# Kernel tuning notes

Measured on AMD Instinct MI355X. Metric: run time of the kernel, lower is better.

The kernel has to match this reference:

```python
import jax, jax.numpy as jnp
import numpy as np

EPS = 1e-5  # torch BatchNorm2d default eps
K = 3       # kernel_size
D = 1       # dilation (== padding)


def setup_inputs() -> dict:
    key = jax.random.key(0)
    k0, k1, k2 = jax.random.split(key, 3)
    N, C, H, W, O = 4, 2048, 32, 32, 256
    return {
        "x": jax.random.normal(k0, (N, C, H, W), jnp.float32),
        "conv_w": jax.random.normal(k1, (K * K, C, K, K), jnp.float32) * 0.01,
        "gamma": jnp.ones((K * K,), jnp.float32),
        "beta": jnp.zeros((K * K,), jnp.float32),
        "weight": jax.random.normal(k2, (O, C, K * K), jnp.float32) * 0.01,
    }


def reference(x, conv_w, gamma, beta, weight):
    n, c, h, w = x.shape
    # --- dynamic-kernel generator: conv (stride 1, pad=dilation) -> BN (train mode) -> softmax over K*K ---
    sigma = jax.lax.conv_general_dilated(
        x, conv_w, window_strides=(1, 1), padding=[(D, D), (D, D)],
        rhs_dilation=(D, D), dimension_numbers=("NCHW", "OIHW", "NCHW"))  # (n, K*K, h, w)
    mean = sigma.mean(axis=(0, 2, 3), keepdims=True)
    var = sigma.var(axis=(0, 2, 3), keepdims=True)  # biased variance, as torch BN uses for normalization
    sigma = (sigma - mean) * jax.lax.rsqrt(var + EPS)
    sigma = sigma * gamma[None, :, None, None] + beta[None, :, None, None]
    sigma = jax.nn.softmax(sigma, axis=1)            # softmax over the K*K kernel positions
    sigma = sigma.reshape(n, K * K, h * w)           # (n, K*K, h*w)
    # --- unfold (im2col), channel-major (C, kh, kw) ordering matching torch F.unfold ---
    patches = jax.lax.conv_general_dilated_patches(
        x, (K, K), (1, 1), [(D, D), (D, D)], rhs_dilation=(D, D),
        dimension_numbers=("NCHW", "OIHW", "NCHW"))  # (n, C*K*K, h, w)
    patches = patches.reshape(n, c, K * K, h * w)     # (n, C, K*K, h*w)
    # --- per-pixel dynamic weighting + learned projection ---
    # out[n,o,m] = sum_{c,l} patches[n,c,l,m] * sigma[n,l,m] * weight[o,c,l]
    out = jnp.einsum("nclm,nlm,ocl->nom", patches, sigma, weight)
    return out.reshape(n, weight.shape[0], h, w)
```

## Files before the change

kernel.cpp:

```cpp
#include <hip/hip_runtime.h>
#include <hip/hip_bf16.h>
#include <stdint.h>

typedef unsigned short u16;
typedef __attribute__((ext_vector_type(8))) short short8;
typedef __attribute__((ext_vector_type(4))) float floatx4;

#define N_IMG 4
#define C_IN  2048
#define HW    1024
#define KK    9
#define O_OUT 256
#define NPIX  4096
#define M_PAD  2432
#define K_DIM  2048
#define BN_EPS 1e-5f

#define OFF_A    0u
#define OFF_XT   9961472u
#define OFF_H    26738688u
#define OFF_SRAW 46661632u
#define OFF_STAT 46809088u

__device__ __forceinline__ u16 f2b(float f) {
    unsigned u = __float_as_uint(f);
    return (u16)((u + 0x7FFFu + ((u >> 16) & 1u)) >> 16);
}

__device__ __forceinline__ void load8f(const float* base, size_t eidx, u16* out) {
    const float* p = base + eidx;
    float4 a = ((const float4*)p)[0];
    float4 b = ((const float4*)p)[1];
    float f[8] = {a.x, a.y, a.z, a.w, b.x, b.y, b.z, b.w};
#pragma unroll
    for (int j = 0; j < 8; ++j) out[j] = f2b(f[j]);
}

__global__ void build_all(const float* __restrict__ x, const float* __restrict__ wgt,
                          const float* __restrict__ cw, u16* __restrict__ xt,
                          u16* __restrict__ A, float* __restrict__ stats) {
    __shared__ __align__(16) u16 lds[9 * 2056];
    int b = blockIdx.x, t = threadIdx.x;
    if (b < 2048) {
        int c0 = (b & 31) * 64, p0 = ((b >> 5) & 15) * 64, n = b >> 9;
        int rp = t >> 3;
        int pv = (t & 7) * 8;
        u16 h0[8], h1[8];
        load8f(x, (size_t)(n * C_IN + c0 + 2 * rp) * HW + p0 + pv, h0);
        load8f(x, (size_t)(n * C_IN + c0 + 2 * rp + 1) * HW + p0 + pv, h1);
        unsigned* l32 = (unsigned*)lds;
#pragma unroll
        for (int j = 0; j < 8; ++j)
            l32[(pv + j) * 35 + rp] = (unsigned)h0[j] | ((unsigned)h1[j] << 16);
        __syncthreads();
        int pr = t >> 3, cq = (t & 7) * 4;
        unsigned o0[4], o1[4];
#pragma unroll
        for (int i = 0; i < 4; ++i) {
            o0[i] = l32[pr * 35 + cq + i];
            o1[i] = l32[(pr + 32) * 35 + cq + i];
        }
        *(uint4*)(xt + (size_t)(n * HW + p0 + pr) * K_DIM + c0 + cq * 2) = *(uint4*)o0;
        *(uint4*)(xt + (size_t)(n * HW + p0 + pr + 32) * K_DIM + c0 + cq * 2) = *(uint4*)o1;
    } else if (b < 2304) {
        int o = b - 2048;
        size_t base = (size_t)o * 18432;
        for (int i = 0; i < 9; ++i) {
            int e0 = (t + i * 256) * 8;
            u16 hv[8];
            load8f(wgt, base + e0, hv);
#pragma unroll
            for (int j = 0; j < 8; ++j) {
                int e = e0 + j;
                int c = e / 9, l = e - c * 9;
                lds[l * 2056 + c] = hv[j];
            }
        }
        __syncthreads();
        for (int l = 0; l < 9; ++l) {
            size_t row = (size_t)l * 256 + o;
            *(uint4*)(A + row * K_DIM + t * 8) = *(const uint4*)&lds[l * 2056 + t * 8];
        }
    } else if (b < 2313) {
        int l = b - 2304;
        size_t base = (size_t)l * 18432;
        for (int i = 0; i < 9; ++i) {
            int e0 = (t + i * 256) * 8;
            u16 hv[8];
            load8f(cw, base + e0, hv);
#pragma unroll
            for (int j = 0; j < 8; ++j) {
                int e = e0 + j;
                int c = e / 9, k = e - c * 9;
                lds[k * 2056 + c] = hv[j];
            }
        }
        __syncthreads();
        for (int k = 0; k < 9; ++k) {
            size_t row = 2304 + (size_t)k * 9 + l;
            *(uint4*)(A + row * K_DIM + t * 8) = *(const uint4*)&lds[k * 2056 + t * 8];
        }
    } else {
        uint4 z = {0, 0, 0, 0};
        uint4* dst = (uint4*)(A + (size_t)2385 * K_DIM);
        for (int i = t; i < (47 * 2048) / 8; i += 256) dst[i] = z;
        if (t < 18) stats[t] = 0.0f;
    }
}

__device__ __forceinline__ void gload_lds16(const void* g, void* l) {
    __builtin_amdgcn_global_load_lds((__attribute__((address_space(1))) void*)(g),
                                     (__attribute__((address_space(3))) void*)(l), 16, 0, 0);
}

__global__ void gemm_bt(const u16* __restrict__ A, const u16* __restrict__ B,
                        __hip_bfloat16* __restrict__ C) {
    __shared__ __align__(16) u16 As[2 * 128 * 32];
    __shared__ __align__(16) u16 Bs[2 * 128 * 32];
    int bx = blockIdx.x;
    int mt = bx % 19, nt = bx / 19;
    int m0 = mt * 128, n0 = nt * 128;
    int t = threadIdx.x;
    int w = t >> 6, lam = t & 63;
    int wm = w >> 1, wn = w & 1;
    int lm = lam & 15, q = lam >> 4;

    floatx4 acc[4][4];
    floatx4 z = {0.f, 0.f, 0.f, 0.f};
#pragma unroll
    for (int i = 0; i < 4; ++i)
#pragma unroll
        for (int j = 0; j < 4; ++j) acc[i][j] = z;

    int rsub = lam >> 2;
    int kc = (lam & 3) * 8;
    const u16* gA[4]; const u16* gB[4];
    u16* lA[4];       u16* lB[4];
#pragma unroll
    for (int ii = 0; ii < 4; ++ii) {
        int c = w * 4 + ii;
        int rc = c & 7, ks = c >> 3;
        gA[ii] = A + (size_t)(m0 + rc * 16 + rsub) * K_DIM + ks * 32 + kc;
        gB[ii] = B + (size_t)(n0 + rc * 16 + rsub) * K_DIM + ks * 32 + kc;
        lA[ii] = As + ks * 4096 + rc * 512;
        lB[ii] = Bs + ks * 4096 + rc * 512;
    }

    for (int kt = 0; kt < K_DIM / 64; ++kt) {
#pragma unroll
        for (int ii = 0; ii < 4; ++ii) {
            gload_lds16(gA[ii], lA[ii]);
            gload_lds16(gB[ii], lB[ii]);
            gA[ii] += 64; gB[ii] += 64;
        }
        __syncthreads();
#pragma unroll
        for (int ks = 0; ks < 2; ++ks) {
            short8 af[4], bf[4];
#pragma unroll
            for (int i = 0; i < 4; ++i)
                af[i] = *(const short8*)(As + ks * 4096 + (wm * 64 + i * 16 + lm) * 32 + q * 8);
#pragma unroll
            for (int j = 0; j < 4; ++j)
                bf[j] = *(const short8*)(Bs + ks * 4096 + (wn * 64 + j * 16 + lm) * 32 + q * 8);
#pragma unroll
            for (int i = 0; i < 4; ++i)
#pragma unroll
                for (int j = 0; j < 4; ++j)
                    acc[i][j] = __builtin_amdgcn_mfma_f32_16x16x32_bf16(af[i], bf[j], acc[i][j], 0, 0, 0);
        }
        __syncthreads();
    }
#pragma unroll
    for (int i = 0; i < 4; ++i) {
        int gm = m0 + wm * 64 + i * 16 + q * 4;
#pragma unroll
        for (int j = 0; j < 4; ++j) {
            int gn = n0 + wn * 64 + j * 16 + lm;
#pragma unroll
            for (int r = 0; r < 4; ++r)
                C[(size_t)(gm + r) * NPIX + gn] = __float2bfloat16(acc[i][j][r]);
        }
    }
}

__global__ void sigma_stats(const __hip_bfloat16* __restrict__ Hm, float* __restrict__ sraw,
                            float* __restrict__ stats) {
    int b = blockIdx.x;
    int qq = b & 3, nl = b >> 2;
    int n = nl / 9, l = nl - n * 9;
    int t = threadIdx.x;
    int pix = qq * 256 + t;
    int y = pix >> 5, x = pix & 31;
    float v = 0.f;
#pragma unroll
    for (int k = 0; k < 9; ++k) {
        int yy = y + k / 3 - 1, xx = x + (k % 3) - 1;
        if (yy >= 0 && yy < 32 && xx >= 0 && xx < 32)
            v += __bfloat162float(Hm[(size_t)(2304 + k * 9 + l) * NPIX + n * HW + yy * 32 + xx]);
    }
    sraw[(size_t)nl * HW + pix] = v;
    __shared__ float r1[256], r2[256];
    r1[t] = v; r2[t] = v * v;
    __syncthreads();
    for (int s = 128; s > 0; s >>= 1) {
        if (t < s) { r1[t] += r1[t + s]; r2[t] += r2[t + s]; }
        __syncthreads();
    }
    if (t == 0) { atomicAdd(&stats[l], r1[0]); atomicAdd(&stats[9 + l], r2[0]); }
}

__global__ void tail(const __hip_bfloat16* __restrict__ Hm, const float* __restrict__ sraw,
                     const float* __restrict__ stats, const float* __restrict__ gamma,
                     const float* __restrict__ beta, float* __restrict__ out) {
    int b = blockIdx.x;
    int n = b >> 8, rem = b & 255;
    int ph = rem >> 7, og = rem & 127;
    int t = threadIdx.x;
    float mean[9], istd[9], gg[9], bb[9];
#pragma unroll
    for (int l = 0; l < 9; ++l) {
        float m = stats[l] * (1.f / 4096.f);
        float var = stats[9 + l] * (1.f / 4096.f) - m * m;
        mean[l] = m; istd[l] = rsqrtf(var + BN_EPS);
        gg[l] = gamma[l]; bb[l] = beta[l];
    }
    const __hip_bfloat16* hb = Hm + (size_t)(og * 2) * NPIX + (size_t)n * HW;
    float* ob = out + ((size_t)n * 256 + og * 2) * HW;
#pragma unroll
    for (int i = 0; i < 2; ++i) {
        int pix = ph * 512 + i * 256 + t;
        int y = pix >> 5, x = pix & 31;
        float v[9];
        float mx = -1e30f;
#pragma unroll
        for (int l = 0; l < 9; ++l) {
            float tv = (sraw[(size_t)(n * 9 + l) * HW + pix] - mean[l]) * istd[l];
            tv = tv * gg[l] + bb[l];
            v[l] = tv; mx = fmaxf(mx, tv);
        }
        float ssum = 0.f;
#pragma unroll
        for (int l = 0; l < 9; ++l) { v[l] = __expf(v[l] - mx); ssum += v[l]; }
        float inv = 1.f / ssum;
        float acc0 = 0.f, acc1 = 0.f;
#pragma unroll
        for (int l = 0; l < 9; ++l) {
            int dy = l / 3 - 1, dx = l % 3 - 1;
            int yy = y + dy, xx = x + dx;
            if (yy >= 0 && yy < 32 && xx >= 0 && xx < 32) {
                float sv = v[l] * inv;
                size_t hidx = (size_t)(l * 256) * NPIX + (size_t)(pix + dy * 32 + dx);
                acc0 += sv * __bfloat162float(hb[hidx]);
                acc1 += sv * __bfloat162float(hb[hidx + NPIX]);
            }
        }
        ob[pix] = acc0;
        ob[HW + pix] = acc1;
    }
}

extern "C" void kernel_launch(void* const* d_in, const int* in_sizes, int n_in,
                              void* d_out, int out_size, void* d_ws, size_t ws_size,
                              hipStream_t stream) {
    const float* x     = (const float*)d_in[0];
    const float* cw    = (const float*)d_in[1];
    const float* gamma = (const float*)d_in[2];
    const float* beta  = (const float*)d_in[3];
    const float* wgt   = (const float*)d_in[4];

    char* ws = (char*)d_ws;
    u16*   Abuf = (u16*)(ws + OFF_A);
    u16*   XT   = (u16*)(ws + OFF_XT);
    u16*   Hm   = (u16*)(ws + OFF_H);
    float* sraw = (float*)(ws + OFF_SRAW);
    float* stats= (float*)(ws + OFF_STAT);

    build_all<<<2314, 256, 0, stream>>>(x, wgt, cw, XT, Abuf, stats);
    gemm_bt<<<19 * 32, 256, 0, stream>>>(Abuf, XT, (__hip_bfloat16*)Hm);
    sigma_stats<<<N_IMG * KK * 4, 256, 0, stream>>>((const __hip_bfloat16*)Hm, sraw, stats);
    tail<<<1024, 256, 0, stream>>>((const __hip_bfloat16*)Hm, sraw, stats, gamma, beta, (float*)d_out);
}
```

Measured before the change: 170.6 us.

## Rewrite GEMM with 256x256 tiles, swizzled LDS and ping-pong pipelined MFMA schedule

```diff
diff --git a/kernel.cpp b/kernel.cpp
--- a/kernel.cpp
+++ b/kernel.cpp
@@ -12,15 +12,16 @@
 #define KK    9
 #define O_OUT 256
 #define NPIX  4096
-#define M_PAD  2432
+#define M_PAD  2560
+#define H_ROWS 2432
 #define K_DIM  2048
 #define BN_EPS 1e-5f
 
 #define OFF_A    0u
-#define OFF_XT   9961472u
-#define OFF_H    26738688u
-#define OFF_SRAW 46661632u
-#define OFF_STAT 46809088u
+#define OFF_XT   10485760u
+#define OFF_H    27262976u
+#define OFF_SRAW 47185920u
+#define OFF_STAT 47333376u
 
 __device__ __forceinline__ u16 f2b(float f) {
     unsigned u = __float_as_uint(f);
@@ -113,73 +114,155 @@
                                      (__attribute__((address_space(3))) void*)(l), 16, 0, 0);
 }
 
-__global__ void gemm_bt(const u16* __restrict__ A, const u16* __restrict__ B,
-                        __hip_bfloat16* __restrict__ C) {
-    __shared__ __align__(16) u16 As[2 * 128 * 32];
-    __shared__ __align__(16) u16 Bs[2 * 128 * 32];
-    int bx = blockIdx.x;
-    int mt = bx % 19, nt = bx / 19;
-    int m0 = mt * 128, n0 = nt * 128;
+#define STG(gbase, ldsarr, bb, hh, kt) do {                                                        \
+    gload_lds16((gbase) + (size_t)((hh) * 128 + (w * 2 + 0) * 8) * K_DIM + (size_t)(kt) * 64,      \
+                (ldsarr) + (bb) * 16384 + (hh) * 8192 + ldsw);                                     \
+    gload_lds16((gbase) + (size_t)((hh) * 128 + (w * 2 + 1) * 8) * K_DIM + (size_t)(kt) * 64,      \
+                (ldsarr) + (bb) * 16384 + (hh) * 8192 + ldsw + 512);                               \
+} while (0)
+
+#define RD_A(bb, mi, ks) (*(const short8*)(As + (bb) * 16384 + arow + (mi) * 1024 + col[ks]))
+#define RD_B(bb, ni, ks) (*(const short8*)(Bs + (bb) * 16384 + brow + (ni) * 1024 + col[ks]))
+
+#define READ_BALL(bb) do {                                                   \
+    bq[0][0] = RD_B(bb, 0, 0); bq[0][1] = RD_B(bb, 0, 1);                    \
+    bq[1][0] = RD_B(bb, 1, 0); bq[1][1] = RD_B(bb, 1, 1);                    \
+    bq[2][0] = RD_B(bb, 2, 0); bq[2][1] = RD_B(bb, 2, 1);                    \
+    bq[3][0] = RD_B(bb, 3, 0); bq[3][1] = RD_B(bb, 3, 1);                    \
+} while (0)
+
+#define READ_AQ(bb, qd) do {                                                 \
+    aq[0][0] = RD_A(bb, 2 * (qd), 0);     aq[0][1] = RD_A(bb, 2 * (qd), 1);  \
+    aq[1][0] = RD_A(bb, 2 * (qd) + 1, 0); aq[1][1] = RD_A(bb, 2 * (qd) + 1, 1); \
+} while (0)
+
+#define MFMA1(mi, ni, ks) acc[mi][ni] = __builtin_amdgcn_mfma_f32_16x16x32_bf16( \
+    aq[(mi) & 1][ks], bq[ni][ks], acc[mi][ni], 0, 0, 0)
+
+#define MFMA_Q(qd) do {                                                                      \
+    MFMA1(2*(qd),   0, 0); MFMA1(2*(qd),   1, 0); MFMA1(2*(qd),   2, 0); MFMA1(2*(qd),   3, 0); \
+    MFMA1(2*(qd)+1, 0, 0); MFMA1(2*(qd)+1, 1, 0); MFMA1(2*(qd)+1, 2, 0); MFMA1(2*(qd)+1, 3, 0); \
+    MFMA1(2*(qd),   0, 1); MFMA1(2*(qd),   1, 1); MFMA1(2*(qd),   2, 1); MFMA1(2*(qd),   3, 1); \
+    MFMA1(2*(qd)+1, 0, 1); MFMA1(2*(qd)+1, 1, 1); MFMA1(2*(qd)+1, 2, 1); MFMA1(2*(qd)+1, 3, 1); \
+} while (0)
+
+#define BAR1_MFMA(qd) do {                                   \
+    __builtin_amdgcn_s_barrier();                            \
+    asm volatile("s_waitcnt lgkmcnt(0)" ::: "memory");       \
+    __builtin_amdgcn_sched_barrier(0);                       \
+    __builtin_amdgcn_s_setprio(1);                           \
+    MFMA_Q(qd);                                              \
+    __builtin_amdgcn_s_setprio(0);                           \
+} while (0)
+#define BAR2() __builtin_amdgcn_s_barrier()
+#define VMW4() asm volatile("s_waitcnt vmcnt(4)" ::: "memory")
+#define VMW0() asm volatile("s_waitcnt vmcnt(0)" ::: "memory")
+
+__global__ __launch_bounds__(512, 2) void gemm_bt(const u16* __restrict__ A,
+                                                  const u16* __restrict__ B,
+                                                  __hip_bfloat16* __restrict__ C) {
+    __shared__ __align__(16) u16 As[2 * 256 * 64];
+    __shared__ __align__(16) u16 Bs[2 * 256 * 64];
+
+    int orig = blockIdx.x;
+    int wgid = (orig & 7) * 20 + (orig >> 3);
+    int mt = wgid % 10, nt = wgid / 10;
+    int m0 = mt * 256, n0 = nt * 256;
+
     int t = threadIdx.x;
-    int w = t >> 6, lam = t & 63;
-    int wm = w >> 1, wn = w & 1;
-    int lm = lam & 15, q = lam >> 4;
-
-    floatx4 acc[4][4];
+    int w = t >> 6, L = t & 63;
+    int wm = w >> 2, wn = w & 3;
+    int q = L >> 4, lm = L & 15;
+    int lr = L >> 3, ls = L & 7;
+
+    int csw = (ls ^ lr) * 8;
+    const u16* gA0 = A + (size_t)(m0 + lr) * K_DIM + csw;
+    const u16* gB0 = B + (size_t)(n0 + lr) * K_DIM + csw;
+    int ldsw = w * 1024;
+
+    int sw = (lm & 7) << 3;
+    int arow = (wm * 128 + lm) * 64;
+    int brow = (wn * 64 + lm) * 64;
+    int col[2] = { (q * 8) ^ sw, (32 + q * 8) ^ sw };
+
+    floatx4 acc[8][4];
     floatx4 z = {0.f, 0.f, 0.f, 0.f};
 #pragma unroll
-    for (int i = 0; i < 4; ++i)
+    for (int i = 0; i < 8; ++i)
 #pragma unroll
         for (int j = 0; j < 4; ++j) acc[i][j] = z;
 
-    int rsub = lam >> 2;
-    int kc = (lam & 3) * 8;
-    const u16* gA[4]; const u16* gB[4];
-    u16* lA[4];       u16* lB[4];
-#pragma unroll
-    for (int ii = 0; ii < 4; ++ii) {
-        int c = w * 4 + ii;
-        int rc = c & 7, ks = c >> 3;
-        gA[ii] = A + (size_t)(m0 + rc * 16 + rsub) * K_DIM + ks * 32 + kc;
-        gB[ii] = B + (size_t)(n0 + rc * 16 + rsub) * K_DIM + ks * 32 + kc;
-        lA[ii] = As + ks * 4096 + rc * 512;
-        lB[ii] = Bs + ks * 4096 + rc * 512;
-    }
-
-    for (int kt = 0; kt < K_DIM / 64; ++kt) {
-#pragma unroll
-        for (int ii = 0; ii < 4; ++ii) {
-            gload_lds16(gA[ii], lA[ii]);
-            gload_lds16(gB[ii], lB[ii]);
-            gA[ii] += 64; gB[ii] += 64;
-        }
-        __syncthreads();
-#pragma unroll
-        for (int ks = 0; ks < 2; ++ks) {
-            short8 af[4], bf[4];
-#pragma unroll
-            for (int i = 0; i < 4; ++i)
-                af[i] = *(const short8*)(As + ks * 4096 + (wm * 64 + i * 16 + lm) * 32 + q * 8);
-#pragma unroll
-            for (int j = 0; j < 4; ++j)
-                bf[j] = *(const short8*)(Bs + ks * 4096 + (wn * 64 + j * 16 + lm) * 32 + q * 8);
-#pragma unroll
-            for (int i = 0; i < 4; ++i)
-#pragma unroll
-                for (int j = 0; j < 4; ++j)
-                    acc[i][j] = __builtin_amdgcn_mfma_f32_16x16x32_bf16(af[i], bf[j], acc[i][j], 0, 0, 0);
-        }
-        __syncthreads();
-    }
-#pragma unroll
-    for (int i = 0; i < 4; ++i) {
-        int gm = m0 + wm * 64 + i * 16 + q * 4;
-#pragma unroll
-        for (int j = 0; j < 4; ++j) {
-            int gn = n0 + wn * 64 + j * 16 + lm;
-#pragma unroll
-            for (int r = 0; r < 4; ++r)
-                C[(size_t)(gm + r) * NPIX + gn] = __float2bfloat16(acc[i][j][r]);
+    short8 aq[2][2], bq[4][2];
+
+    STG(gA0, As, 0, 0, 0); STG(gA0, As, 0, 1, 0);
+    STG(gB0, Bs, 0, 0, 0); STG(gB0, Bs, 0, 1, 0);
+    STG(gB0, Bs, 1, 0, 1); STG(gB0, Bs, 1, 1, 1);
+    VMW4();
+    BAR2();
+
+    for (int it = 0; it < 15; ++it) {
+        int T = 2 * it;
+        READ_BALL(0); READ_AQ(0, 0);
+        STG(gA0, As, 1, 0, T + 1); STG(gA0, As, 1, 1, T + 1);
+        BAR1_MFMA(0); BAR2();
+        READ_AQ(0, 1);
+        STG(gB0, Bs, 0, 0, T + 2);
+        BAR1_MFMA(1); BAR2();
+        READ_AQ(0, 2);
+        STG(gB0, Bs, 0, 1, T + 2);
+        BAR1_MFMA(2); BAR2();
+        READ_AQ(0, 3);
+        BAR1_MFMA(3); VMW4(); BAR2();
+        READ_BALL(1); READ_AQ(1, 0);
+        STG(gA0, As, 0, 0, T + 2); STG(gA0, As, 0, 1, T + 2);
+        BAR1_MFMA(0); BAR2();
+        READ_AQ(1, 1);
+        STG(gB0, Bs, 1, 0, T + 3);
+        BAR1_MFMA(1); BAR2();
+        READ_AQ(1, 2);
+        STG(gB0, Bs, 1, 1, T + 3);
+        BAR1_MFMA(2); BAR2();
+        READ_AQ(1, 3);
+        BAR1_MFMA(3); VMW4(); BAR2();
+    }
+
+    READ_BALL(0); READ_AQ(0, 0);
+    STG(gA0, As, 1, 0, 31); STG(gA0, As, 1, 1, 31);
+    BAR1_MFMA(0); BAR2();
+    READ_AQ(0, 1); BAR1_MFMA(1); BAR2();
+    READ_AQ(0, 2); BAR1_MFMA(2); BAR2();
+    READ_AQ(0, 3); BAR1_MFMA(3); VMW0(); BAR2();
+    READ_BALL(1); READ_AQ(1, 0); BAR1_MFMA(0); BAR2();
+    READ_AQ(1, 1); BAR1_MFMA(1); BAR2();
+    READ_AQ(1, 2); BAR1_MFMA(2); BAR2();
+    READ_AQ(1, 3); BAR1_MFMA(3); BAR2();
+
+    if (m0 + 255 < H_ROWS) {
+#pragma unroll
+        for (int mi = 0; mi < 8; ++mi) {
+            int gm = m0 + wm * 128 + mi * 16 + q * 4;
+#pragma unroll
+            for (int ni = 0; ni < 4; ++ni) {
+                int gn = n0 + wn * 64 + ni * 16 + lm;
+#pragma unroll
+                for (int r = 0; r < 4; ++r)
+                    C[(size_t)(gm + r) * NPIX + gn] = __float2bfloat16(acc[mi][ni][r]);
+            }
+        }
+    } else {
+#pragma unroll
+        for (int mi = 0; mi < 8; ++mi) {
+            int gm = m0 + wm * 128 + mi * 16 + q * 4;
+#pragma unroll
+            for (int ni = 0; ni < 4; ++ni) {
+                int gn = n0 + wn * 64 + ni * 16 + lm;
+#pragma unroll
+                for (int r = 0; r < 4; ++r) {
+                    int row = gm + r;
+                    if (row < H_ROWS)
+                        C[(size_t)row * NPIX + gn] = __float2bfloat16(acc[mi][ni][r]);
+                }
+            }
         }
     }
 }
@@ -277,7 +360,7 @@
     float* stats= (float*)(ws + OFF_STAT);
 
     build_all<<<2314, 256, 0, stream>>>(x, wgt, cw, XT, Abuf, stats);
-    gemm_bt<<<19 * 32, 256, 0, stream>>>(Abuf, XT, (__hip_bfloat16*)Hm);
+    gemm_bt<<<160, 512, 0, stream>>>(Abuf, XT, (__hip_bfloat16*)Hm);
     sigma_stats<<<N_IMG * KK * 4, 256, 0, stream>>>((const __hip_bfloat16*)Hm, sraw, stats);
     tail<<<1024, 256, 0, stream>>>((const __hip_bfloat16*)Hm, sraw, stats, gamma, beta, (float*)d_out);
 }
```

Result: no change. 173.8 us (+1.8%).
